# Optimization experiments

Measured on AMD Instinct MI355X. Metric: run time of the kernel, lower is better.

The kernel has to match this reference:

```python
import jax, jax.numpy as jnp
import numpy as np

EYE_PENALTY = 1.0e6


def setup_inputs() -> dict:
    key = jax.random.key(0)
    k1, k2 = jax.random.split(key)
    B, NIN, NK, DK = 512, 1024, 128, 5
    x = jax.random.normal(k1, (B, NIN), dtype=jnp.float32)
    theta = jax.random.normal(k2, (NIN, NK, DK), dtype=jnp.float32) * 0.05
    log_weight_scale = jnp.zeros((NK, DK), dtype=jnp.float32)
    bias = jnp.full((NK,), -1.0, dtype=jnp.float32)
    return {"x": x, "theta": theta, "log_weight_scale": log_weight_scale, "bias": bias}


def reference(x, theta, log_weight_scale, bias):
    # kernel = theta * exp(log_weight_scale) / ||theta||_2 (norm over input dim)
    l2 = jnp.sqrt(jnp.sum(theta * theta, axis=0))            # [K, D]
    kernel = theta * (jnp.exp(log_weight_scale) / l2)[None]   # [NIN, K, D]
    actv = jnp.einsum('bi,ikd->bkd', x, kernel)               # [B, K, D]
    B = x.shape[0]
    # all-pairs L1 distance per kernel: [B, K, B]
    diff = actv[:, :, :, None] - jnp.transpose(actv, (1, 2, 0))[None]  # [B,K,D,B]
    abs_dif = jnp.sum(jnp.abs(diff), axis=2)                  # [B, K, B]
    abs_dif = abs_dif + EYE_PENALTY * jnp.eye(B, dtype=x.dtype)[:, None, :]
    f = jnp.sum(jnp.exp(-abs_dif), axis=2) + bias[None, :]    # [B, K]
    return jnp.concatenate([x, f], axis=1)                    # [B, NIN + K]
```

## Files before the change

### kernel.cpp

```cpp
#include <hip/hip_runtime.h>
#include <hip/hip_fp16.h>
#include <math.h>

constexpr int B    = 512;
constexpr int NIN  = 1024;
constexpr int NK   = 128;
constexpr int DK   = 5;
constexpr int NF   = NK * DK;
constexpr int NOUT = NIN + NK;
constexpr int SPLITK = 8;
constexpr int LDA = 136;
#define LOG2E 1.44269504088896f

typedef _Float16 f16x4 __attribute__((ext_vector_type(4)));
typedef _Float16 f16x8 __attribute__((ext_vector_type(8)));
typedef float    f32x4 __attribute__((ext_vector_type(4)));

__global__ __launch_bounds__(256) void gemm_kernel(
        const float* __restrict__ x,
        const float* __restrict__ theta,
        __half* __restrict__ actvP16,
        float* __restrict__ ps) {
    __shared__ _Float16 Ath[32 * LDA];
    __shared__ _Float16 Bxh[64 * LDA];
    __shared__ float    red2[32][33];

    const int t    = threadIdx.x;
    const int tile = blockIdx.x >> 3;
    const int z    = blockIdx.x & 7;
    const int nt   = tile >> 3;
    const int bt   = tile & 7;
    const int n0   = nt * 32;
    const int b0   = bt * 64;
    const bool do_ps = (bt == 0);
    const int kw   = z * 128;

    const int kq = t >> 3;
    const int nc = (t & 7) * 4;
    float4 tv0 = *(const float4*)&theta[(kw + kq*4 + 0) * NF + n0 + nc];
    float4 tv1 = *(const float4*)&theta[(kw + kq*4 + 1) * NF + n0 + nc];
    float4 tv2 = *(const float4*)&theta[(kw + kq*4 + 2) * NF + n0 + nc];
    float4 tv3 = *(const float4*)&theta[(kw + kq*4 + 3) * NF + n0 + nc];

    const int br = t >> 2;
    const int ki = t & 3;
    float4 xv[8];
    #pragma unroll
    for (int i = 0; i < 8; ++i)
        xv[i] = *(const float4*)&x[(b0 + br) * NIN + kw + (ki + i * 4) * 4];

    if (do_ps) {
        red2[kq][nc + 0] = tv0.x*tv0.x + tv1.x*tv1.x + tv2.x*tv2.x + tv3.x*tv3.x;
        red2[kq][nc + 1] = tv0.y*tv0.y + tv1.y*tv1.y + tv2.y*tv2.y + tv3.y*tv3.y;
        red2[kq][nc + 2] = tv0.z*tv0.z + tv1.z*tv1.z + tv2.z*tv2.z + tv3.z*tv3.z;
        red2[kq][nc + 3] = tv0.w*tv0.w + tv1.w*tv1.w + tv2.w*tv2.w + tv3.w*tv3.w;
    }

    {
        f16x4 h;
        h[0]=(_Float16)tv0.x; h[1]=(_Float16)tv1.x; h[2]=(_Float16)tv2.x; h[3]=(_Float16)tv3.x;
        *(f16x4*)&Ath[(nc + 0) * LDA + kq * 4] = h;
        h[0]=(_Float16)tv0.y; h[1]=(_Float16)tv1.y; h[2]=(_Float16)tv2.y; h[3]=(_Float16)tv3.y;
        *(f16x4*)&Ath[(nc + 1) * LDA + kq * 4] = h;
        h[0]=(_Float16)tv0.z; h[1]=(_Float16)tv1.z; h[2]=(_Float16)tv2.z; h[3]=(_Float16)tv3.z;
        *(f16x4*)&Ath[(nc + 2) * LDA + kq * 4] = h;
        h[0]=(_Float16)tv0.w; h[1]=(_Float16)tv1.w; h[2]=(_Float16)tv2.w; h[3]=(_Float16)tv3.w;
        *(f16x4*)&Ath[(nc + 3) * LDA + kq * 4] = h;
    }
    #pragma unroll
    for (int i = 0; i < 8; ++i) {
        f16x4 h;
        h[0] = (_Float16)xv[i].x;  h[1] = (_Float16)xv[i].y;
        h[2] = (_Float16)xv[i].z;  h[3] = (_Float16)xv[i].w;
        *(f16x4*)&Bxh[br * LDA + (ki + i * 4) * 4] = h;
    }
    __syncthreads();

    const int w   = t >> 6;
    const int l   = t & 63;
    const int r16 = l & 15;
    const int kg  = l >> 4;

    f32x4 acc0 = {0.f,0.f,0.f,0.f}, acc1 = {0.f,0.f,0.f,0.f};
    #pragma unroll
    for (int ks = 0; ks < 4; ++ks) {
        const f16x8 bv  = *(const f16x8*)&Bxh[(w*16 + r16)*LDA + ks*32 + kg*8];
        const f16x8 av0 = *(const f16x8*)&Ath[( 0 + r16)*LDA + ks*32 + kg*8];
        const f16x8 av1 = *(const f16x8*)&Ath[(16 + r16)*LDA + ks*32 + kg*8];
        acc0 = __builtin_amdgcn_mfma_f32_16x16x32_f16(av0, bv, acc0, 0, 0, 0);
        acc1 = __builtin_amdgcn_mfma_f32_16x16x32_f16(av1, bv, acc1, 0, 0, 0);
    }

    {
        __half* dst = actvP16 + (size_t)z * NF * B
                    + (size_t)(n0 + kg*4) * B + b0 + w*16 + r16;
        #pragma unroll
        for (int j = 0; j < 4; ++j) {
            dst[j*B]          = __float2half(acc0[j]);
            dst[(16 + j) * B] = __float2half(acc1[j]);
        }
    }
    if (do_ps) {
        __syncthreads();
        if (t < 32) {
            float tot = 0.f;
            #pragma unroll
            for (int rr = 0; rr < 32; ++rr) tot += red2[rr][t];
            ps[z * NF + n0 + t] = tot;
        }
    }
}

__global__ __launch_bounds__(1024, 4) void pairwise_kernel(
        const __half* __restrict__ actvP16,
        const float* __restrict__ ps,
        const float* __restrict__ lws,
        const float* __restrict__ bias,
        const float* __restrict__ x,
        float* __restrict__ out) {
    __shared__ __half a16s[DK * B];
    __shared__ float  red[16 * 256];
    __shared__ float  s_sh[DK];
    __shared__ float  red_ps[DK * SPLITK];

    const int k = blockIdx.x;
    const int e = blockIdx.y;
    const int t = threadIdx.x;

    if (t >= 512) {
        const int u = t - 512;
        const int row = k * 4 + e * 2 + (u >> 8);
        const int c4  = u & 255;
        ((float4*)out)[row * (NOUT/4) + c4] = ((const float4*)x)[row * (NIN/4) + c4];
    }
    if (t >= 320 && t < 320 + DK * SPLITK) {
        const int u = t - 320;
        red_ps[u] = ps[(u / DK) * NF + k * DK + (u % DK)];
    }

    const size_t slab = (size_t)k * DK * B;
    float accf[8];
    #pragma unroll
    for (int i = 0; i < 8; ++i) accf[i] = 0.f;
    if (t < 320) {
        #pragma unroll
        for (int z = 0; z < SPLITK; ++z) {
            const f16x8 v = *(const f16x8*)(actvP16 + (size_t)z * NF * B + slab + t * 8);
            #pragma unroll
            for (int i = 0; i < 8; ++i) accf[i] += (float)v[i];
        }
    }
    __syncthreads();
    if (t < DK) {
        float sum = 0.f;
        #pragma unroll
        for (int c = 0; c < SPLITK; ++c) sum += red_ps[c * DK + t];
        s_sh[t] = __expf(lws[k * DK + t]) * rsqrtf(sum) * LOG2E;
    }
    __syncthreads();
    if (t < 320) {
        const float s = s_sh[t >> 6];
        f16x8 h;
        #pragma unroll
        for (int i = 0; i < 8; ++i) h[i] = (_Float16)(accf[i] * s);
        *(f16x8*)&a16s[t * 8] = h;
    }
    __syncthreads();

    const int w  = t >> 6;
    const int l  = t & 63;
    const int ba = e * 256 + l * 4;

    __half2 A2[4][DK];
    #pragma unroll
    for (int j = 0; j < 4; ++j)
        #pragma unroll
        for (int d = 0; d < DK; ++d)
            A2[j][d] = __half2half2(a16s[d * B + ba + j]);

    float acc[4] = {0.f, 0.f, 0.f, 0.f};
    const int bp0 = w * 32;

    union W8 { f16x8 v; __half2 h[4]; };
    #pragma unroll
    for (int m = 0; m < 4; ++m) {
        const int bp = bp0 + m * 8;
        W8 w0, w1, w2, w3, w4;
        w0.v = *(const f16x8*)&a16s[0*B + bp];
        w1.v = *(const f16x8*)&a16s[1*B + bp];
        w2.v = *(const f16x8*)&a16s[2*B + bp];
        w3.v = *(const f16x8*)&a16s[3*B + bp];
        w4.v = *(const f16x8*)&a16s[4*B + bp];
        #pragma unroll
        for (int c = 0; c < 4; ++c) {
            #pragma unroll
            for (int j = 0; j < 4; ++j) {
                __half2 dA = __habs2(__hsub2(A2[j][0], w0.h[c]));
                dA = __hadd2(dA, __habs2(__hsub2(A2[j][1], w1.h[c])));
                dA = __hadd2(dA, __habs2(__hsub2(A2[j][2], w2.h[c])));
                dA = __hadd2(dA, __habs2(__hsub2(A2[j][3], w3.h[c])));
                dA = __hadd2(dA, __habs2(__hsub2(A2[j][4], w4.h[c])));
                const float lo = __low2float(dA);
                const float hi = __high2float(dA);
                acc[j] += __builtin_amdgcn_exp2f(-lo);
                acc[j] += __builtin_amdgcn_exp2f(-hi);
            }
        }
    }
    #pragma unroll
    for (int j = 0; j < 4; ++j)
        red[w * 256 + (l * 4 + j)] = acc[j];
    __syncthreads();

    if (t < 256) {
        float f = -1.0f + bias[k];
        #pragma unroll
        for (int gg = 0; gg < 16; ++gg) f += red[gg * 256 + t];
        out[(size_t)(e * 256 + t) * NOUT + NIN + k] = f;
    }
}

extern "C" void kernel_launch(void* const* d_in, const int* in_sizes, int n_in,
                              void* d_out, int out_size, void* d_ws, size_t ws_size,
                              hipStream_t stream) {
    const float* x     = (const float*)d_in[0];
    const float* theta = (const float*)d_in[1];
    const float* lws   = (const float*)d_in[2];
    const float* bias  = (const float*)d_in[3];
    float* out = (float*)d_out;

    char* wsb = (char*)d_ws;
    float*  ps       = (float*)wsb;
    __half* actvP16  = (__half*)(wsb + (64 << 10));

    gemm_kernel<<<dim3(1280), 256, 0, stream>>>(x, theta, actvP16, ps);
    pairwise_kernel<<<dim3(NK, 2), 1024, 0, stream>>>(actvP16, ps, lws, bias, x, out);
}
```

Measured before the change: 24.63 us.

## Exploit pairwise distance symmetry to halve exp work in pairwise kernel

The pairwise L1 kernel now computes only the lower-triangular half of the 512x512 distance matrix per feature. Each exp term is added to both a row sum and a column sum, using shared-memory atomics, wave shuffles and a masked diagonal. Exponentials are evaluated in packed half precision (h2exp2) and reduced with fdot2. Bias initialization moves into the GEMM kernel, and the two blocks per feature combine their partial results with global atomics. This roughly halves the exp and ALU work, at the cost of atomic traffic, load imbalance across waves, fp16 accumulation of column sums, and nondeterministic summation order.

```diff
diff --git a/kernel.cpp b/kernel.cpp
--- a/kernel.cpp
+++ b/kernel.cpp
@@ -12,6 +12,7 @@
 constexpr int LDA = 136;
 #define LOG2E 1.44269504088896f
 
+typedef _Float16 f16x2v __attribute__((ext_vector_type(2)));
 typedef _Float16 f16x4 __attribute__((ext_vector_type(4)));
 typedef _Float16 f16x8 __attribute__((ext_vector_type(8)));
 typedef float    f32x4 __attribute__((ext_vector_type(4)));
@@ -19,8 +20,10 @@
 __global__ __launch_bounds__(256) void gemm_kernel(
         const float* __restrict__ x,
         const float* __restrict__ theta,
+        const float* __restrict__ bias,
         __half* __restrict__ actvP16,
-        float* __restrict__ ps) {
+        float* __restrict__ ps,
+        float* __restrict__ out) {
     __shared__ _Float16 Ath[32 * LDA];
     __shared__ _Float16 Bxh[64 * LDA];
     __shared__ float    red2[32][33];
@@ -34,6 +37,13 @@
     const int b0   = bt * 64;
     const bool do_ps = (bt == 0);
     const int kw   = z * 128;
+
+    if (blockIdx.x < 256) {
+        const int u   = blockIdx.x * 256 + t;
+        const int row = u >> 7;
+        const int col = u & 127;
+        out[(size_t)row * NOUT + NIN + col] = bias[col];
+    }
 
     const int kq = t >> 3;
     const int nc = (t & 7) * 4;
@@ -115,21 +125,24 @@
         const __half* __restrict__ actvP16,
         const float* __restrict__ ps,
         const float* __restrict__ lws,
-        const float* __restrict__ bias,
         const float* __restrict__ x,
         float* __restrict__ out) {
     __shared__ __half a16s[DK * B];
-    __shared__ float  red[16 * 256];
+    __shared__ float  rowsum[B];
+    __shared__ float  colsum[B];
     __shared__ float  s_sh[DK];
     __shared__ float  red_ps[DK * SPLITK];
 
     const int k = blockIdx.x;
-    const int e = blockIdx.y;
+    const int h = blockIdx.y;
     const int t = threadIdx.x;
 
-    if (t >= 512) {
+    if (t < 512) {
+        rowsum[t] = 0.f;
+    } else {
+        colsum[t - 512] = 0.f;
         const int u = t - 512;
-        const int row = k * 4 + e * 2 + (u >> 8);
+        const int row = k * 4 + 2 * h + (u >> 8);
         const int c4  = u & 255;
         ((float4*)out)[row * (NOUT/4) + c4] = ((const float4*)x)[row * (NIN/4) + c4];
     }
@@ -160,64 +173,96 @@
     __syncthreads();
     if (t < 320) {
         const float s = s_sh[t >> 6];
-        f16x8 h;
-        #pragma unroll
-        for (int i = 0; i < 8; ++i) h[i] = (_Float16)(accf[i] * s);
-        *(f16x8*)&a16s[t * 8] = h;
-    }
-    __syncthreads();
-
-    const int w  = t >> 6;
-    const int l  = t & 63;
-    const int ba = e * 256 + l * 4;
-
-    __half2 A2[4][DK];
-    #pragma unroll
-    for (int j = 0; j < 4; ++j)
+        f16x8 hv;
+        #pragma unroll
+        for (int i = 0; i < 8; ++i) hv[i] = (_Float16)(accf[i] * s);
+        *(f16x8*)&a16s[t * 8] = hv;
+    }
+    __syncthreads();
+
+    const int w = t >> 6;
+    const int l = t & 63;
+    const int W = h * 16 + w;
+
+    union W8 { f16x8 v; __half2 h2[4]; };
+    union HU { __half2 h; unsigned u; };
+
+    #pragma unroll
+    for (int jj = 0; jj < 2; ++jj) {
+        const int j  = jj ? (63 - W) : W;
+        const int c0 = j * 8;
+        W8 cd[5];
         #pragma unroll
         for (int d = 0; d < DK; ++d)
-            A2[j][d] = __half2half2(a16s[d * B + ba + j]);
-
-    float acc[4] = {0.f, 0.f, 0.f, 0.f};
-    const int bp0 = w * 32;
-
-    union W8 { f16x8 v; __half2 h[4]; };
-    #pragma unroll
-    for (int m = 0; m < 4; ++m) {
-        const int bp = bp0 + m * 8;
-        W8 w0, w1, w2, w3, w4;
-        w0.v = *(const f16x8*)&a16s[0*B + bp];
-        w1.v = *(const f16x8*)&a16s[1*B + bp];
-        w2.v = *(const f16x8*)&a16s[2*B + bp];
-        w3.v = *(const f16x8*)&a16s[3*B + bp];
-        w4.v = *(const f16x8*)&a16s[4*B + bp];
-        #pragma unroll
-        for (int c = 0; c < 4; ++c) {
-            #pragma unroll
-            for (int j = 0; j < 4; ++j) {
-                __half2 dA = __habs2(__hsub2(A2[j][0], w0.h[c]));
-                dA = __hadd2(dA, __habs2(__hsub2(A2[j][1], w1.h[c])));
-                dA = __hadd2(dA, __habs2(__hsub2(A2[j][2], w2.h[c])));
-                dA = __hadd2(dA, __habs2(__hsub2(A2[j][3], w3.h[c])));
-                dA = __hadd2(dA, __habs2(__hsub2(A2[j][4], w4.h[c])));
-                const float lo = __low2float(dA);
-                const float hi = __high2float(dA);
-                acc[j] += __builtin_amdgcn_exp2f(-lo);
-                acc[j] += __builtin_amdgcn_exp2f(-hi);
+            cd[d].v = *(const f16x8*)&a16s[d * B + c0];
+
+        HU ca[4];
+        ca[0].u = 0u; ca[1].u = 0u; ca[2].u = 0u; ca[3].u = 0u;
+
+        const int mstrip = j >> 3;
+        const int q = l - 8 * (j & 7);
+        for (int i = 0; i <= mstrip; ++i) {
+            const int r = i * 64 + l;
+            __half2 A2[DK];
+            #pragma unroll
+            for (int d = 0; d < DK; ++d)
+                A2[d] = __half2half2(a16s[d * B + r]);
+            const bool diag = (i == mstrip);
+            float rowacc = 0.f;
+            #pragma unroll
+            for (int s = 0; s < 4; ++s) {
+                __half2 dA = __habs2(__hsub2(A2[0], cd[0].h2[s]));
+                dA = __hadd2(dA, __habs2(__hsub2(A2[1], cd[1].h2[s])));
+                dA = __hadd2(dA, __habs2(__hsub2(A2[2], cd[2].h2[s])));
+                dA = __hadd2(dA, __habs2(__hsub2(A2[3], cd[3].h2[s])));
+                dA = __hadd2(dA, __habs2(__hsub2(A2[4], cd[4].h2[s])));
+                HU e; e.h = h2exp2(__hneg2(dA));
+                if (diag) {
+                    HU m;
+                    m.u = ((2*s     > q) ? 0x00003C00u : 0u)
+                        | ((2*s + 1 > q) ? 0x3C000000u : 0u);
+                    e.h = __hmul2(e.h, m.h);
+                }
+#if __has_builtin(__builtin_amdgcn_fdot2)
+                {
+                    HU ones; ones.u = 0x3C003C00u;
+                    rowacc = __builtin_amdgcn_fdot2(
+                        *(f16x2v*)&e.u, *(f16x2v*)&ones.u, rowacc, false);
+                }
+#else
+                rowacc += __low2float(e.h) + __high2float(e.h);
+#endif
+                ca[s].h = __hadd2(ca[s].h, e.h);
             }
-        }
-    }
-    #pragma unroll
-    for (int j = 0; j < 4; ++j)
-        red[w * 256 + (l * 4 + j)] = acc[j];
-    __syncthreads();
-
-    if (t < 256) {
-        float f = -1.0f + bias[k];
-        #pragma unroll
-        for (int gg = 0; gg < 16; ++gg) f += red[gg * 256 + t];
-        out[(size_t)(e * 256 + t) * NOUT + NIN + k] = f;
-    }
+            atomicAdd(&rowsum[r], rowacc);
+        }
+
+        float c0f = __low2float(ca[0].h), c1f = __high2float(ca[0].h);
+        float c2f = __low2float(ca[1].h), c3f = __high2float(ca[1].h);
+        float c4f = __low2float(ca[2].h), c5f = __high2float(ca[2].h);
+        float c6f = __low2float(ca[3].h), c7f = __high2float(ca[3].h);
+        #pragma unroll
+        for (int msk = 1; msk < 64; msk <<= 1) {
+            c0f += __shfl_xor(c0f, msk, 64);
+            c1f += __shfl_xor(c1f, msk, 64);
+            c2f += __shfl_xor(c2f, msk, 64);
+            c3f += __shfl_xor(c3f, msk, 64);
+            c4f += __shfl_xor(c4f, msk, 64);
+            c5f += __shfl_xor(c5f, msk, 64);
+            c6f += __shfl_xor(c6f, msk, 64);
+            c7f += __shfl_xor(c7f, msk, 64);
+        }
+        if (l < 8) {
+            const float v = (l == 0) ? c0f : (l == 1) ? c1f : (l == 2) ? c2f :
+                            (l == 3) ? c3f : (l == 4) ? c4f : (l == 5) ? c5f :
+                            (l == 6) ? c6f : c7f;
+            atomicAdd(&colsum[c0 + l], v);
+        }
+    }
+    __syncthreads();
+
+    if (t < 512)
+        atomicAdd(&out[(size_t)t * NOUT + NIN + k], rowsum[t] + colsum[t]);
 }
 
 extern "C" void kernel_launch(void* const* d_in, const int* in_sizes, int n_in,
@@ -233,6 +278,6 @@
     float*  ps       = (float*)wsb;
     __half* actvP16  = (__half*)(wsb + (64 << 10));
 
-    gemm_kernel<<<dim3(1280), 256, 0, stream>>>(x, theta, actvP16, ps);
-    pairwise_kernel<<<dim3(NK, 2), 1024, 0, stream>>>(actvP16, ps, lws, bias, x, out);
+    gemm_kernel<<<dim3(1280), 256, 0, stream>>>(x, theta, bias, actvP16, ps, out);
+    pairwise_kernel<<<dim3(NK, 2), 1024, 0, stream>>>(actvP16, ps, lws, x, out);
 }
```

After: 41.82 us. +69.8%, slower.
